# Optimization experiments

Measured on AMD Instinct MI355X. Metric: run time of the kernel, lower is better.

The kernel has to match this reference:

```python
import jax, jax.numpy as jnp
import numpy as np

HIDDEN = 1024
HEADS = 16
HEAD_DIM = HIDDEN // HEADS          # 64
ROT = 2 * (HEAD_DIM // 3 // 2)      # 20 (d/h/w rotary chunk), residual = 4
GRID = 256 // 16                    # crop_size // patch_size = 16
DEPTH = 16 // 2                     # frames_per_clip // tubelet_size = 8
N_VIDEO = DEPTH * GRID * GRID       # 2048
N_ACTION = 16
B = 2
SCALE = HEAD_DIM ** -0.5


def _rope(x, pos):
    # interleaved RoPE (VJEPA2 rotate_queries_or_keys): pairs (x[2i], x[2i+1])
    D = x.shape[-1]
    omega = 1.0 / (10000.0 ** (jnp.arange(D // 2, dtype=x.dtype) / (D / 2.0)))
    freq = pos.astype(x.dtype)[..., None] * omega          # (N, D/2)
    cos, sin = jnp.cos(freq), jnp.sin(freq)
    x1, x2 = x[..., 0::2], x[..., 1::2]
    return jnp.stack([x1 * cos - x2 * sin, x2 * cos + x1 * sin], axis=-1).reshape(x.shape)


def _rope3(qk, d_pos, h_pos, w_pos):
    # rotate three ROT-sized chunks (depth/height/width axes), leave residual dims as-is
    parts = [_rope(qk[..., 0:ROT], d_pos),
             _rope(qk[..., ROT:2 * ROT], h_pos),
             _rope(qk[..., 2 * ROT:3 * ROT], w_pos)]
    if 3 * ROT < HEAD_DIM:
        parts.append(qk[..., 3 * ROT:])
    return jnp.concatenate(parts, axis=-1)


def _forward(video_hidden_states, action_hidden_states, W_q, b_q, W_k, b_k, W_v, b_v,
             W_qa, b_qa, W_ka, b_ka, W_va, b_va, W_proj, b_proj, W_proj_a, b_proj_a):
    Bsz, Nv, _ = video_hidden_states.shape
    Na = action_hidden_states.shape[1]

    def proj(x, W, b):  # -> (B, H, N, Dh)
        y = x @ W.T + b
        return y.reshape(Bsz, -1, HEADS, HEAD_DIM).transpose(0, 2, 1, 3)

    qv = proj(video_hidden_states, W_q, b_q)
    kv = proj(video_hidden_states, W_k, b_k)
    vv = proj(video_hidden_states, W_v, b_v)

    # 3-axis position ids for raster-ordered video tokens
    ids = jnp.arange(Nv)
    tpf = GRID * GRID
    d_pos = ids // tpf
    rem = ids - tpf * d_pos
    h_pos = rem // GRID
    w_pos = rem - GRID * h_pos

    qv = _rope3(qv, d_pos, h_pos, w_pos)
    kv = _rope3(kv, d_pos, h_pos, w_pos)

    qa = proj(action_hidden_states, W_qa, b_qa)
    ka = proj(action_hidden_states, W_ka, b_ka)
    va = proj(action_hidden_states, W_va, b_va)

    # actions: linspace between frame-id of token 0 and token 1 (faithful to source)
    a_pos = jnp.linspace(d_pos[0].astype(jnp.float32), d_pos[1].astype(jnp.float32), Na)
    qa = _rope3(qa, a_pos, a_pos, a_pos)
    ka = _rope3(ka, a_pos, a_pos, a_pos)

    # joint attention over concatenated video+action token sequence
    q = jnp.concatenate([qv, qa], axis=2)
    k = jnp.concatenate([kv, ka], axis=2)
    v = jnp.concatenate([vv, va], axis=2)

    scores = jnp.einsum('bhqd,bhkd->bhqk', q, k) * SCALE
    probs = jax.nn.softmax(scores, axis=-1)
    ctx = jnp.einsum('bhqk,bhkd->bhqd', probs, v)
    ctx = ctx.transpose(0, 2, 1, 3).reshape(Bsz, Nv + Na, HIDDEN)

    out_video = ctx[:, :Nv] @ W_proj.T + b_proj
    out_action = ctx[:, Nv:] @ W_proj_a.T + b_proj_a
    return out_video, out_action


def setup_inputs() -> dict:
    key = jax.random.key(0)
    ks = jax.random.split(key, 12)
    sd = HIDDEN ** -0.5
    inp = {}
    for i, n in enumerate(['q', 'k', 'v', 'qa', 'ka', 'va', 'proj', 'proj_a']):
        inp[f'W_{n}'] = jax.random.normal(ks[i], (HIDDEN, HIDDEN), jnp.float32) * sd
        inp[f'b_{n}'] = jnp.zeros((HIDDEN,), jnp.float32)
    inp['video_hidden_states'] = jax.random.normal(ks[10], (B, N_VIDEO, HIDDEN), jnp.float32)
    inp['action_hidden_states'] = jax.random.normal(ks[11], (B, N_ACTION, HIDDEN), jnp.float32)
    return inp


def reference(video_hidden_states, action_hidden_states, W_q, b_q, W_k, b_k, W_v, b_v,
              W_qa, b_qa, W_ka, b_ka, W_va, b_va, W_proj, b_proj, W_proj_a, b_proj_a):
    return _forward(video_hidden_states, action_hidden_states, W_q, b_q, W_k, b_k, W_v, b_v,
                    W_qa, b_qa, W_ka, b_ka, W_va, b_va, W_proj, b_proj, W_proj_a, b_proj_a)
```

## Files before the change

### kernel.cpp

```cpp
#include <hip/hip_runtime.h>
#include <stdint.h>

#define HID   1024
#define NHEAD 16
#define HDIM  64
#define NV    2048
#define NA    16
#define NTOK  2064
#define BSZ   2
#define MROWS 4128
#define MPAD  4224
#define WSZ   1048576
#define EXP_C1 0.18033688011112042f
#define EXP_C2 16.0f

#define POFF(r,k)  (((((r)>>4)*32  + ((k)>>5))*512) + ((((k)>>3)&3)*128) + (((r)&15)*8) + ((k)&7))
#define QOFF(t,d)  (((((t)>>4)*2   + ((d)>>5))*512) + ((((d)>>3)&3)*128) + (((t)&15)*8) + ((d)&7))
#define VOFF(d,ky) (((((d)>>4)*65  + ((ky)>>5))*512) + ((((ky)>>3)&3)*128) + (((d)&15)*8) + ((ky)&7))
#define QPLANE (129*2*512)
#define VPLANE (4*65*512)

typedef __bf16 bf16x8 __attribute__((ext_vector_type(8)));
typedef unsigned short u16x8 __attribute__((ext_vector_type(8)));
typedef unsigned short u16x4 __attribute__((ext_vector_type(4)));
typedef float f32x4 __attribute__((ext_vector_type(4)));

__device__ __forceinline__ unsigned short f2bf(float f) {
  unsigned u = __builtin_bit_cast(unsigned, f);
  u += 0x7FFFu + ((u >> 16) & 1u);
  return (unsigned short)(u >> 16);
}
__device__ __forceinline__ float bf2f_trunc_inv(unsigned short h) {
  unsigned u = ((unsigned)h) << 16; return __builtin_bit_cast(float, u);
}
__device__ __forceinline__ unsigned short f2bf_trunc(float f) {
  return (unsigned short)(__builtin_bit_cast(unsigned, f) >> 16);
}
__device__ __forceinline__ bf16x8 ldfrag(const unsigned short* p) {
  return __builtin_bit_cast(bf16x8, *(const u16x8*)p);
}

__global__ __launch_bounds__(256) void cvt_kernel(
    const float* __restrict__ W0, const float* __restrict__ W1,
    const float* __restrict__ W2, const float* __restrict__ W3,
    const float* __restrict__ W4, const float* __restrict__ W5,
    const float* __restrict__ W6, const float* __restrict__ W7,
    const float* __restrict__ video, const float* __restrict__ action,
    unsigned short* __restrict__ Wb, unsigned short* __restrict__ Xp)
{
  const int y = blockIdx.y;
  const size_t idx = ((size_t)blockIdx.x * 256 + threadIdx.x) * 8;
  const float* src; unsigned short* dstbase; int row;
  if (y < 8) {
    const float* Ws[8] = {W0, W1, W2, W3, W4, W5, W6, W7};
    src = Ws[y] + idx; dstbase = Wb + (size_t)y * WSZ; row = (int)(idx >> 10);
  } else if (y < 12) {
    src = video + (size_t)(y - 8) * WSZ + idx; dstbase = Xp;
    row = ((y - 8) << 10) + (int)(idx >> 10);
  } else {
    if (idx >= (size_t)BSZ * NA * HID) return;
    src = action + idx; dstbase = Xp; row = 4096 + (int)(idx >> 10);
  }
  const int k0 = (int)(idx & 1023);
  float4 f0 = *(const float4*)src;
  float4 f1 = *(const float4*)(src + 4);
  u16x8 v;
  v[0]=f2bf(f0.x); v[1]=f2bf(f0.y); v[2]=f2bf(f0.z); v[3]=f2bf(f0.w);
  v[4]=f2bf(f1.x); v[5]=f2bf(f1.y); v[6]=f2bf(f1.z); v[7]=f2bf(f1.w);
  *(u16x8*)(dstbase + POFF(row, k0)) = v;
}

__device__ __forceinline__ void row2bt(int rg, int& b, int& tok, bool& valid) {
  if (rg < 4096) { b = rg >> 11; tok = rg & 2047; valid = true; }
  else { int t = rg - 4096; b = t >> 4; tok = 2048 + (t & 15); valid = rg < MROWS; }
}

__global__ __launch_bounds__(256) void qkv_kernel(
    const unsigned short* __restrict__ Xp, const unsigned short* __restrict__ Wb,
    const float* __restrict__ bq, const float* __restrict__ bk,
    const float* __restrict__ bv, const float* __restrict__ bqa,
    const float* __restrict__ bka, const float* __restrict__ bva,
    unsigned short* __restrict__ Qpk, unsigned short* __restrict__ Kpk,
    unsigned short* __restrict__ Vpk)
{
  const int tid  = threadIdx.x;
  const int w    = tid >> 6;
  const int lane = tid & 63;
  const int quad = lane >> 4;
  const int l16  = lane & 15;
  const int z    = blockIdx.z;
  const int m0   = blockIdx.y * 128;
  const int n0   = blockIdx.x * 128;
  const bool atile = (blockIdx.y == 32);

  const unsigned short* Wz = Wb + (size_t)(atile ? 3 + z : z) * WSZ;
  const float* bias = (z == 0) ? (atile ? bqa : bq)
                    : (z == 1) ? (atile ? bka : bk)
                               : (atile ? bva : bv);

  const int am = (w & 1) * 64;
  const int bn = (w >> 1) * 64;
  const int Mt = (m0 >> 4) + (am >> 4);
  const int Nt = (n0 >> 4) + (bn >> 4);

  const unsigned short* pa = Xp + (size_t)Mt * 32 * 512 + lane * 8;
  const unsigned short* pb = Wz + (size_t)Nt * 32 * 512 + lane * 8;

  f32x4 acc[4][4] = {};

#pragma unroll 2
  for (int kt = 0; kt < 32; kt++) {
    bf16x8 af[4], bf[4];
#pragma unroll
    for (int mi = 0; mi < 4; mi++) af[mi] = ldfrag(pa + (size_t)(mi * 32 + kt) * 512);
#pragma unroll
    for (int ni = 0; ni < 4; ni++) bf[ni] = ldfrag(pb + (size_t)(ni * 32 + kt) * 512);
#pragma unroll
    for (int mi = 0; mi < 4; mi++)
#pragma unroll
      for (int ni = 0; ni < 4; ni++)
        acc[mi][ni] = __builtin_amdgcn_mfma_f32_16x16x32_bf16(af[mi], bf[ni], acc[mi][ni], 0, 0, 0);
  }

  if (z < 2) {
    unsigned short* O = (z == 0) ? Qpk : Kpk;
#pragma unroll
    for (int mi = 0; mi < 4; mi++) {
      const int rgb = m0 + am + mi * 16 + quad * 4;
#pragma unroll
      for (int ni = 0; ni < 4; ni++) {
        const int gcol = n0 + bn + ni * 16 + l16;
        const int head = gcol >> 6, col = gcol & 63;
        const float bias_v = bias[gcol];
        const int seg = (col >= 40) ? 2 : (col >= 20) ? 1 : 0;
        const int tin = col - seg * 20;
        const float om = exp2f(-(float)(tin >> 1) * 1.3287712379549449f);
        const bool evn = !(tin & 1);
#pragma unroll
        for (int r = 0; r < 4; r++) {
          int rg = rgb + r;
          int b, tok; bool valid;
          row2bt(rg, b, tok, valid);
          float val = acc[mi][ni][r] + bias_v;
          float part = __shfl_xor(val, 1);
          if (tok < 2048 && col < 60) {
            int dp = tok >> 8, hp = (tok >> 4) & 15, wp = tok & 15;
            float pos = (seg == 0) ? (float)dp : (seg == 1) ? (float)hp : (float)wp;
            float fr = pos * om;
            float cs = cosf(fr), sn = sinf(fr);
            val = evn ? (val * cs - part * sn) : (val * cs + part * sn);
          }
          if (valid)
            O[(size_t)(b * NHEAD + head) * QPLANE + QOFF(tok, col)] = f2bf(val);
        }
      }
    }
  } else {
#pragma unroll
    for (int mi = 0; mi < 4; mi++) {
      const int rgb = m0 + am + mi * 16 + quad * 4;
      int b, tok; bool valid;
      row2bt(rgb, b, tok, valid);
#pragma unroll
      for (int ni = 0; ni < 4; ni++) {
        const int gcol = n0 + bn + ni * 16 + l16;
        const int head = gcol >> 6, d = gcol & 63;
        const float bias_v = bias[gcol];
        u16x4 pk;
#pragma unroll
        for (int r = 0; r < 4; r++) pk[r] = f2bf(acc[z >= 2 ? 0 : 0, mi][ni][r] + bias_v);
        if (valid)
          *(u16x4*)&Vpk[(size_t)(b * NHEAD + head) * VPLANE + VOFF(d, tok)] = pk;
      }
    }
  }
}

__global__ __launch_bounds__(256) void attn_kernel(
    const unsigned short* __restrict__ Qpk,
    const unsigned short* __restrict__ Kpk,
    const unsigned short* __restrict__ Vpk,
    unsigned short* __restrict__ ctxp)
{
  __shared__ unsigned short Ps[4][16][68];

  const int tid  = threadIdx.x;
  const int wave = tid >> 6;
  const int lane = tid & 63;
  const int quad = lane >> 4;
  const int l16  = lane & 15;
  const int bh   = blockIdx.y;
  const int q0   = blockIdx.x * 64;
  const unsigned short* Qp = Qpk + (size_t)bh * QPLANE + lane * 8;
  const unsigned short* Kp = Kpk + (size_t)bh * QPLANE + lane * 8;
  const unsigned short* Vp = Vpk + (size_t)bh * VPLANE + lane * 8;

  const int qt = min((q0 >> 4) + wave, 128);
  bf16x8 aq[2];
#pragma unroll
  for (int c = 0; c < 2; c++) aq[c] = ldfrag(Qp + (size_t)(qt * 2 + c) * 512);

  u16x8 ones_u;
#pragma unroll
  for (int i = 0; i < 8; i++) ones_u[i] = 0x3F80;
  const bf16x8 ones = __builtin_bit_cast(bf16x8, ones_u);

  f32x4 oacc[4] = {};
  f32x4 lacc = {};

  for (int it = 0; it < 32; it++) {
    f32x4 sacc[4] = {};
#pragma unroll
    for (int nt = 0; nt < 4; nt++) {
#pragma unroll
      for (int c = 0; c < 2; c++) {
        bf16x8 bk = ldfrag(Kp + (size_t)((it * 4 + nt) * 2 + c) * 512);
        sacc[nt] = __builtin_amdgcn_mfma_f32_16x16x32_bf16(aq[c], bk, sacc[nt], 0, 0, 0);
      }
    }
#pragma unroll
    for (int nt = 0; nt < 4; nt++)
#pragma unroll
      for (int rr = 0; rr < 4; rr++)
        Ps[wave][quad * 4 + rr][nt * 16 + l16] =
            f2bf_trunc(exp2f(__builtin_fmaf(sacc[nt][rr], EXP_C1, -EXP_C2)));

#pragma unroll
    for (int c = 0; c < 2; c++) {
      u16x4 alo = *(const u16x4*)&Ps[wave][l16][c * 32 + quad * 8];
      u16x4 ahi = *(const u16x4*)&Ps[wave][l16][c * 32 + quad * 8 + 4];
      bf16x8 ap = __builtin_bit_cast(bf16x8,
          __builtin_shufflevector(alo, ahi, 0, 1, 2, 3, 4, 5, 6, 7));
#pragma unroll
      for (int nt = 0; nt < 4; nt++) {
        bf16x8 bv = ldfrag(Vp + (size_t)(nt * 65 + it * 2 + c) * 512);
        oacc[nt] = __builtin_amdgcn_mfma_f32_16x16x32_bf16(ap, bv, oacc[nt], 0, 0, 0);
      }
      lacc = __builtin_amdgcn_mfma_f32_16x16x32_bf16(ap, ones, lacc, 0, 0, 0);
    }
  }

  {
    f32x4 s0 = {};
#pragma unroll
    for (int c = 0; c < 2; c++) {
      bf16x8 bk = ldfrag(Kp + (size_t)(128 * 2 + c) * 512);
      s0 = __builtin_amdgcn_mfma_f32_16x16x32_bf16(aq[c], bk, s0, 0, 0, 0);
    }
#pragma unroll
    for (int rr = 0; rr < 4; rr++) {
      Ps[wave][quad * 4 + rr][l16]      = f2bf_trunc(exp2f(__builtin_fmaf(s0[rr], EXP_C1, -EXP_C2)));
      Ps[wave][quad * 4 + rr][16 + l16] = 0;
    }
    u16x4 alo = *(const u16x4*)&Ps[wave][l16][quad * 8];
    u16x4 ahi = *(const u16x4*)&Ps[wave][l16][quad * 8 + 4];
    bf16x8 ap = __builtin_bit_cast(bf16x8,
        __builtin_shufflevector(alo, ahi, 0, 1, 2, 3, 4, 5, 6, 7));
#pragma unroll
    for (int nt = 0; nt < 4; nt++) {
      bf16x8 bv = ldfrag(Vp + (size_t)(nt * 65 + 64) * 512);
      oacc[nt] = __builtin_amdgcn_mfma_f32_16x16x32_bf16(ap, bv, oacc[nt], 0, 0, 0);
    }
    lacc = __builtin_amdgcn_mfma_f32_16x16x32_bf16(ap, ones, lacc, 0, 0, 0);
  }

  const int b = bh >> 4, h = bh & 15;
  float rl[4];
#pragma unroll
  for (int rr = 0; rr < 4; rr++) rl[rr] = 1.f / lacc[rr];
#pragma unroll
  for (int nt = 0; nt < 4; nt++) {
#pragma unroll
    for (int rr = 0; rr < 4; rr++) {
      int token = q0 + wave * 16 + quad * 4 + rr;
      if (token < NTOK) {
        int row = (token < 2048) ? (b * 2048 + token) : (4096 + b * NA + (token - 2048));
        int col = h * HDIM + nt * 16 + l16;
        ctxp[POFF(row, col)] = f2bf(oacc[nt][rr] * rl[rr]);
      }
    }
  }
}

__global__ __launch_bounds__(256) void proj_kernel(
    const unsigned short* __restrict__ ctxp, const unsigned short* __restrict__ Wb,
    const float* __restrict__ bp, const float* __restrict__ bpa,
    float* __restrict__ out)
{
  const int tid  = threadIdx.x;
  const int w    = tid >> 6;
  const int lane = tid & 63;
  const int quad = lane >> 4;
  const int l16  = lane & 15;
  const int m0   = blockIdx.y * 128;
  const int n0   = blockIdx.x * 128;
  const bool atile = (blockIdx.y == 32);

  const unsigned short* Wz = Wb + (size_t)(atile ? 7 : 6) * WSZ;
  const float* bias = atile ? bpa : bp;

  const int am = (w & 1) * 64;
  const int bn = (w >> 1) * 64;
  const int Mt = (m0 >> 4) + (am >> 4);
  const int Nt = (n0 >> 4) + (bn >> 4);

  const unsigned short* pa = ctxp + (size_t)Mt * 32 * 512 + lane * 8;
  const unsigned short* pb = Wz + (size_t)Nt * 32 * 512 + lane * 8;

  f32x4 acc[4][4] = {};

#pragma unroll 2
  for (int kt = 0; kt < 32; kt++) {
    bf16x8 af[4], bf[4];
#pragma unroll
    for (int mi = 0; mi < 4; mi++) af[mi] = ldfrag(pa + (size_t)(mi * 32 + kt) * 512);
#pragma unroll
    for (int ni = 0; ni < 4; ni++) bf[ni] = ldfrag(pb + (size_t)(ni * 32 + kt) * 512);
#pragma unroll
    for (int mi = 0; mi < 4; mi++)
#pragma unroll
      for (int ni = 0; ni < 4; ni++)
        acc[mi][ni] = __builtin_amdgcn_mfma_f32_16x16x32_bf16(af[mi], bf[ni], acc[mi][ni], 0, 0, 0);
  }

#pragma unroll
  for (int mi = 0; mi < 4; mi++) {
    const int rgb = m0 + am + mi * 16 + quad * 4;
#pragma unroll
    for (int ni = 0; ni < 4; ni++) {
      const int gcol = n0 + bn + ni * 16 + l16;
      const float bias_v = bias[gcol];
#pragma unroll
      for (int r = 0; r < 4; r++) {
        int rg = rgb + r;
        if (rg < MROWS) out[(size_t)rg * HID + gcol] = acc[mi][ni][r] + bias_v;
      }
    }
  }
}

extern "C" void kernel_launch(void* const* d_in, const int* in_sizes, int n_in,
                              void* d_out, int out_size, void* d_ws, size_t ws_size,
                              hipStream_t stream) {
  const float* A[18];
  if (in_sizes[0] == HID * HID) {
    for (int i = 0; i < 18; i++) A[i] = (const float*)d_in[i];
  } else {
    A[16] = (const float*)d_in[0];
    A[17] = (const float*)d_in[1];
    for (int i = 0; i < 16; i++) A[i] = (const float*)d_in[i + 2];
  }
  const float *Wq = A[0], *bq = A[1], *Wk = A[2], *bk = A[3], *Wv = A[4], *bv = A[5];
  const float *Wqa = A[6], *bqa = A[7], *Wka = A[8], *bka = A[9], *Wva = A[10], *bva = A[11];
  const float *Wp = A[12], *bp = A[13], *Wpa = A[14], *bpa = A[15];
  const float *video = A[16], *action = A[17];
  float* out = (float*)d_out;

  unsigned short* Wb   = (unsigned short*)d_ws;
  unsigned short* Xp   = Wb + (size_t)8 * WSZ;
  unsigned short* Qpk  = Xp + (size_t)(MPAD / 16) * 32 * 512;
  unsigned short* Kpk  = Qpk + (size_t)32 * QPLANE;
  unsigned short* Vpk  = Kpk + (size_t)32 * QPLANE;
  unsigned short* ctxp = Vpk + (size_t)32 * VPLANE;

  dim3 g0(512, 13);
  cvt_kernel<<<g0, 256, 0, stream>>>(Wq, Wk, Wv, Wqa, Wka, Wva, Wp, Wpa,
                                     video, action, Wb, Xp);
  dim3 g1(8, 33, 3);
  qkv_kernel<<<g1, 256, 0, stream>>>(Xp, Wb, bq, bk, bv, bqa, bka, bva,
                                     Qpk, Kpk, Vpk);
  dim3 g2(33, BSZ * NHEAD);
  attn_kernel<<<g2, 256, 0, stream>>>(Qpk, Kpk, Vpk, ctxp);
  dim3 g3(8, 33);
  proj_kernel<<<g3, 256, 0, stream>>>(ctxp, Wb, bp, bpa, out);
}
```

Before: 359.3 us.

## Shrink per-wave GEMM tiles, double-buffer fragment loads, reorder qkv grid

```diff
diff --git a/kernel.cpp b/kernel.cpp
--- a/kernel.cpp
+++ b/kernel.cpp
@@ -29,9 +29,6 @@
   unsigned u = __builtin_bit_cast(unsigned, f);
   u += 0x7FFFu + ((u >> 16) & 1u);
   return (unsigned short)(u >> 16);
-}
-__device__ __forceinline__ float bf2f_trunc_inv(unsigned short h) {
-  unsigned u = ((unsigned)h) << 16; return __builtin_bit_cast(float, u);
 }
 __device__ __forceinline__ unsigned short f2bf_trunc(float f) {
   return (unsigned short)(__builtin_bit_cast(unsigned, f) >> 16);
@@ -75,7 +72,7 @@
   else { int t = rg - 4096; b = t >> 4; tok = 2048 + (t & 15); valid = rg < MROWS; }
 }
 
-__global__ __launch_bounds__(256) void qkv_kernel(
+__global__ __launch_bounds__(512) void qkv_kernel(
     const unsigned short* __restrict__ Xp, const unsigned short* __restrict__ Wb,
     const float* __restrict__ bq, const float* __restrict__ bk,
     const float* __restrict__ bv, const float* __restrict__ bqa,
@@ -88,48 +85,54 @@
   const int lane = tid & 63;
   const int quad = lane >> 4;
   const int l16  = lane & 15;
-  const int z    = blockIdx.z;
-  const int m0   = blockIdx.y * 128;
+  const int mh   = w & 3;
+  const int nh   = w >> 2;
   const int n0   = blockIdx.x * 128;
-  const bool atile = (blockIdx.y == 32);
+  const int z    = blockIdx.y;
+  const int m0   = blockIdx.z * 128;
+  const bool atile = (blockIdx.z == 32);
 
   const unsigned short* Wz = Wb + (size_t)(atile ? 3 + z : z) * WSZ;
   const float* bias = (z == 0) ? (atile ? bqa : bq)
                     : (z == 1) ? (atile ? bka : bk)
                                : (atile ? bva : bv);
 
-  const int am = (w & 1) * 64;
-  const int bn = (w >> 1) * 64;
-  const int Mt = (m0 >> 4) + (am >> 4);
-  const int Nt = (n0 >> 4) + (bn >> 4);
-
+  const int Mt = (m0 >> 4) + mh * 2;
+  const int Nt = (n0 >> 4) + nh * 4;
   const unsigned short* pa = Xp + (size_t)Mt * 32 * 512 + lane * 8;
   const unsigned short* pb = Wz + (size_t)Nt * 32 * 512 + lane * 8;
 
-  f32x4 acc[4][4] = {};
-
-#pragma unroll 2
+  f32x4 acc[2][4] = {};
+  bf16x8 af[2][2], bf[2][4];
+
+#pragma unroll
+  for (int mi = 0; mi < 2; mi++) af[0][mi] = ldfrag(pa + (size_t)(mi * 32) * 512);
+#pragma unroll
+  for (int ni = 0; ni < 4; ni++) bf[0][ni] = ldfrag(pb + (size_t)(ni * 32) * 512);
+
   for (int kt = 0; kt < 32; kt++) {
-    bf16x8 af[4], bf[4];
-#pragma unroll
-    for (int mi = 0; mi < 4; mi++) af[mi] = ldfrag(pa + (size_t)(mi * 32 + kt) * 512);
-#pragma unroll
-    for (int ni = 0; ni < 4; ni++) bf[ni] = ldfrag(pb + (size_t)(ni * 32 + kt) * 512);
-#pragma unroll
-    for (int mi = 0; mi < 4; mi++)
+    const int cb = kt & 1, nb = cb ^ 1;
+    if (kt < 31) {
+#pragma unroll
+      for (int mi = 0; mi < 2; mi++) af[nb][mi] = ldfrag(pa + (size_t)(mi * 32 + kt + 1) * 512);
+#pragma unroll
+      for (int ni = 0; ni < 4; ni++) bf[nb][ni] = ldfrag(pb + (size_t)(ni * 32 + kt + 1) * 512);
+    }
+#pragma unroll
+    for (int mi = 0; mi < 2; mi++)
 #pragma unroll
       for (int ni = 0; ni < 4; ni++)
-        acc[mi][ni] = __builtin_amdgcn_mfma_f32_16x16x32_bf16(af[mi], bf[ni], acc[mi][ni], 0, 0, 0);
+        acc[mi][ni] = __builtin_amdgcn_mfma_f32_16x16x32_bf16(af[cb][mi], bf[cb][ni], acc[mi][ni], 0, 0, 0);
   }
 
   if (z < 2) {
     unsigned short* O = (z == 0) ? Qpk : Kpk;
 #pragma unroll
-    for (int mi = 0; mi < 4; mi++) {
-      const int rgb = m0 + am + mi * 16 + quad * 4;
+    for (int mi = 0; mi < 2; mi++) {
+      const int rgb = m0 + mh * 32 + mi * 16 + quad * 4;
 #pragma unroll
       for (int ni = 0; ni < 4; ni++) {
-        const int gcol = n0 + bn + ni * 16 + l16;
+        const int gcol = n0 + nh * 64 + ni * 16 + l16;
         const int head = gcol >> 6, col = gcol & 63;
         const float bias_v = bias[gcol];
         const int seg = (col >= 40) ? 2 : (col >= 20) ? 1 : 0;
@@ -157,18 +160,18 @@
     }
   } else {
 #pragma unroll
-    for (int mi = 0; mi < 4; mi++) {
-      const int rgb = m0 + am + mi * 16 + quad * 4;
+    for (int mi = 0; mi < 2; mi++) {
+      const int rgb = m0 + mh * 32 + mi * 16 + quad * 4;
       int b, tok; bool valid;
       row2bt(rgb, b, tok, valid);
 #pragma unroll
       for (int ni = 0; ni < 4; ni++) {
-        const int gcol = n0 + bn + ni * 16 + l16;
+        const int gcol = n0 + nh * 64 + ni * 16 + l16;
         const int head = gcol >> 6, d = gcol & 63;
         const float bias_v = bias[gcol];
         u16x4 pk;
 #pragma unroll
-        for (int r = 0; r < 4; r++) pk[r] = f2bf(acc[z >= 2 ? 0 : 0, mi][ni][r] + bias_v);
+        for (int r = 0; r < 4; r++) pk[r] = f2bf(acc[mi][ni][r] + bias_v);
         if (valid)
           *(u16x4*)&Vpk[(size_t)(b * NHEAD + head) * VPLANE + VOFF(d, tok)] = pk;
       }
@@ -292,43 +295,49 @@
   const int lane = tid & 63;
   const int quad = lane >> 4;
   const int l16  = lane & 15;
-  const int m0   = blockIdx.y * 128;
-  const int n0   = blockIdx.x * 128;
-  const bool atile = (blockIdx.y == 32);
+  const int mh   = w & 1;
+  const int nh   = w >> 1;
+  const int m0   = blockIdx.y * 64;
+  const int n0   = blockIdx.x * 64;
+  const bool atile = (blockIdx.y >= 64);
 
   const unsigned short* Wz = Wb + (size_t)(atile ? 7 : 6) * WSZ;
   const float* bias = atile ? bpa : bp;
 
-  const int am = (w & 1) * 64;
-  const int bn = (w >> 1) * 64;
-  const int Mt = (m0 >> 4) + (am >> 4);
-  const int Nt = (n0 >> 4) + (bn >> 4);
-
+  const int Mt = (m0 >> 4) + mh * 2;
+  const int Nt = (n0 >> 4) + nh * 2;
   const unsigned short* pa = ctxp + (size_t)Mt * 32 * 512 + lane * 8;
   const unsigned short* pb = Wz + (size_t)Nt * 32 * 512 + lane * 8;
 
-  f32x4 acc[4][4] = {};
-
-#pragma unroll 2
+  f32x4 acc[2][2] = {};
+  bf16x8 af[2][2], bf[2][2];
+
+#pragma unroll
+  for (int mi = 0; mi < 2; mi++) af[0][mi] = ldfrag(pa + (size_t)(mi * 32) * 512);
+#pragma unroll
+  for (int ni = 0; ni < 2; ni++) bf[0][ni] = ldfrag(pb + (size_t)(ni * 32) * 512);
+
   for (int kt = 0; kt < 32; kt++) {
-    bf16x8 af[4], bf[4];
-#pragma unroll
-    for (int mi = 0; mi < 4; mi++) af[mi] = ldfrag(pa + (size_t)(mi * 32 + kt) * 512);
-#pragma unroll
-    for (int ni = 0; ni < 4; ni++) bf[ni] = ldfrag(pb + (size_t)(ni * 32 + kt) * 512);
-#pragma unroll
-    for (int mi = 0; mi < 4; mi++)
-#pragma unroll
-      for (int ni = 0; ni < 4; ni++)
-        acc[mi][ni] = __builtin_amdgcn_mfma_f32_16x16x32_bf16(af[mi], bf[ni], acc[mi][ni], 0, 0, 0);
-  }
-
-#pragma unroll
-  for (int mi = 0; mi < 4; mi++) {
-    const int rgb = m0 + am + mi * 16 + quad * 4;
-#pragma unroll
-    for (int ni = 0; ni < 4; ni++) {
-      const int gcol = n0 + bn + ni * 16 + l16;
+    const int cb = kt & 1, nb = cb ^ 1;
+    if (kt < 31) {
+#pragma unroll
+      for (int mi = 0; mi < 2; mi++) af[nb][mi] = ldfrag(pa + (size_t)(mi * 32 + kt + 1) * 512);
+#pragma unroll
+      for (int ni = 0; ni < 2; ni++) bf[nb][ni] = ldfrag(pb + (size_t)(ni * 32 + kt + 1) * 512);
+    }
+#pragma unroll
+    for (int mi = 0; mi < 2; mi++)
+#pragma unroll
+      for (int ni = 0; ni < 2; ni++)
+        acc[mi][ni] = __builtin_amdgcn_mfma_f32_16x16x32_bf16(af[cb][mi], bf[cb][ni], acc[mi][ni], 0, 0, 0);
+  }
+
+#pragma unroll
+  for (int mi = 0; mi < 2; mi++) {
+    const int rgb = m0 + mh * 32 + mi * 16 + quad * 4;
+#pragma unroll
+    for (int ni = 0; ni < 2; ni++) {
+      const int gcol = n0 + nh * 32 + ni * 16 + l16;
       const float bias_v = bias[gcol];
 #pragma unroll
       for (int r = 0; r < 4; r++) {
@@ -366,11 +375,11 @@
   dim3 g0(512, 13);
   cvt_kernel<<<g0, 256, 0, stream>>>(Wq, Wk, Wv, Wqa, Wka, Wva, Wp, Wpa,
                                      video, action, Wb, Xp);
-  dim3 g1(8, 33, 3);
-  qkv_kernel<<<g1, 256, 0, stream>>>(Xp, Wb, bq, bk, bv, bqa, bka, bva,
+  dim3 g1(8, 3, 33);
+  qkv_kernel<<<g1, 512, 0, stream>>>(Xp, Wb, bq, bk, bv, bqa, bka, bva,
                                      Qpk, Kpk, Vpk);
   dim3 g2(33, BSZ * NHEAD);
   attn_kernel<<<g2, 256, 0, stream>>>(Qpk, Kpk, Vpk, ctxp);
-  dim3 g3(8, 33);
+  dim3 g3(16, 66);
   proj_kernel<<<g3, 256, 0, stream>>>(ctxp, Wb, bp, bpa, out);
 }
```

Result: faster. 324.0 us (-9.8%).
